# Kernel tuning notes

Measured on AMD Instinct MI355X. Metric: run time of the kernel, lower is better.

Reference implementation:

```python
import jax, jax.numpy as jnp
import numpy as np

N_NODES = 100000
N_EDGES = 1600000
D_FEAT = 128
UNITS = 128
LEAKY_ALPHA = 0.2  # tf.nn.leaky_relu default


def setup_inputs() -> dict:
    key = jax.random.key(0)
    k1, k2, k3, k4 = jax.random.split(key, 4)
    node_states = jax.random.normal(k1, (N_NODES, D_FEAT), dtype=jnp.float32)
    edges = jax.random.randint(k2, (N_EDGES, 2), 0, N_NODES, dtype=jnp.int64)
    kernel = jax.random.normal(k3, (D_FEAT, UNITS), dtype=jnp.float32) * (1.0 / np.sqrt(D_FEAT))
    kernel_attention = jax.random.normal(k4, (2 * UNITS, 1), dtype=jnp.float32) * (1.0 / np.sqrt(2 * UNITS))
    return {
        "node_states": node_states,
        "edges": edges,
        "kernel": kernel,
        "kernel_attention": kernel_attention,
    }


def reference(node_states, edges, kernel, kernel_attention):
    n = node_states.shape[0]
    tgt_idx = edges[:, 0]
    src_idx = edges[:, 1]

    # node_states_transformed: [N, units]
    h = node_states @ kernel

    # Attention logits. concat([tgt, src]) @ ka == tgt @ ka_t + src @ ka_s
    # (avoids materializing the [E, 2*units] concat).
    ka_t = kernel_attention[:UNITS, 0]   # [units]
    ka_s = kernel_attention[UNITS:, 0]   # [units]
    score_t = h @ ka_t                   # [N]
    score_s = h @ ka_s                   # [N]
    e = score_t[tgt_idx] + score_s[src_idx]              # [E]
    e = jax.nn.leaky_relu(e, negative_slope=LEAKY_ALPHA)
    e = jnp.exp(jnp.clip(e, -2.0, 2.0))

    # Segment softmax over incoming edges of each target node.
    sum_e = jax.ops.segment_sum(e, tgt_idx, num_segments=n)  # [N]
    attention = e / (sum_e[tgt_idx] + 1e-9)                  # [E]

    # Weighted scatter-sum of source messages.
    messages = h[src_idx] * attention[:, None]               # [E, units]
    output = jax.ops.segment_sum(messages, tgt_idx, num_segments=n)  # [N, units]
    return output
```

## Files before the change

kernel.cpp:

```cpp
#include <hip/hip_runtime.h>
#include <stdint.h>

typedef unsigned short ushort_t;
typedef __attribute__((ext_vector_type(8))) short short8;
typedef __attribute__((ext_vector_type(4))) float float4v;
typedef __attribute__((ext_vector_type(2))) float float2v;

#define N_NODES 100000
#define N_EDGES 1600000
#define D 128
#define NB_GEMM 1563
#define NBG     521
#define NB_B1   250
#define EPB     6400
#define BUCKETS 782
#define CAP     2560

static __device__ __forceinline__ float2v up2(uint32_t u) {
    float2v r;
    r.x = __builtin_bit_cast(float, u << 16);
    r.y = __builtin_bit_cast(float, u & 0xffff0000u);
    return r;
}
static __device__ __forceinline__ uint32_t f2bf_u(float f) {
    uint32_t u = __builtin_bit_cast(uint32_t, f);
    return (u + 0x7fffu + ((u >> 16) & 1u)) >> 16;
}
static __device__ __forceinline__ ushort_t f2bf(float f) {
    return (ushort_t)f2bf_u(f);
}
static __device__ __forceinline__ uint32_t pack2(float a, float b) {
    return f2bf_u(a) | (f2bf_u(b) << 16);
}
static __device__ __forceinline__ float edge_e(float s) {
    float x = (s >= 0.0f) ? s : 0.2f * s;
    x = fminf(fmaxf(x, -2.0f), 2.0f);
    return __expf(x);
}

__global__ void __launch_bounds__(256) fused_kernel(const float* __restrict__ X,
                                                    const float* __restrict__ W,
                                                    const float* __restrict__ KA,
                                                    ushort_t* __restrict__ H,
                                                    float* __restrict__ st,
                                                    float* __restrict__ ss,
                                                    int M,
                                                    const int* __restrict__ E,
                                                    int* __restrict__ sortedE,
                                                    ushort_t* __restrict__ bmat,
                                                    ushort_t* __restrict__ lofs) {
    __shared__ __align__(16) ushort_t lds_raw[16384];
    __shared__ float lds_wa[256];
    __shared__ int   ldet;
    int tid = threadIdx.x;
    if (blockIdx.x >= NBG) {
        int eb = blockIdx.x - NBG;
        int* lhist = (int*)lds_raw;
        int* lpart = ((int*)lds_raw) + 1024;
        int t = tid;
        if (t == 0) ldet = 0;
        for (int j = t; j < 1024; j += 256) lhist[j] = 0;
        __syncthreads();
        int nz = 0;
#pragma unroll
        for (int j = 0; j < 8; j++)
            if (E[(t + j * 256) * 2 + 1] != 0) nz = 1;
        if (nz) atomicOr(&ldet, 1);
        __syncthreads();
        int i64 = (ldet == 0) ? 1 : 0;
        int base = eb * EPB;
        int bin[25], w[25];
#pragma unroll
        for (int j = 0; j < 25; j++) {
            int i = base + j * 256 + t;
            int tgt, src;
            if (i64) { uint4 v = *(const uint4*)(E + (size_t)i * 4); tgt = (int)v.x; src = (int)v.z; }
            else     { uint2 v = *(const uint2*)(E + (size_t)i * 2); tgt = (int)v.x; src = (int)v.y; }
            if ((unsigned)tgt >= (unsigned)N_NODES) tgt = 0;
            if ((unsigned)src >= (unsigned)N_NODES) src = 0;
            bin[j] = tgt >> 7;
            w[j]   = ((tgt & 127) << 17) | src;
            atomicAdd(&lhist[bin[j]], 1);
        }
        __syncthreads();
        int c0 = lhist[t * 4], c1 = lhist[t * 4 + 1];
        int c2 = lhist[t * 4 + 2], c3 = lhist[t * 4 + 3];
        int sum = c0 + c1 + c2 + c3;
        lpart[t] = sum;
        __syncthreads();
        for (int off = 1; off < 256; off <<= 1) {
            int x = (t >= off) ? lpart[t - off] : 0;
            __syncthreads();
            lpart[t] += x;
            __syncthreads();
        }
        int e0 = lpart[t] - sum;
        int e1 = e0 + c0, e2 = e1 + c1, e3 = e2 + c2;
        int cc[4] = {c0, c1, c2, c3};
        int ee[4] = {e0, e1, e2, e3};
#pragma unroll
        for (int k = 0; k < 4; k++) {
            int bb = t * 4 + k;
            if (bb < BUCKETS) {
                bmat[eb * BUCKETS + bb] = (ushort_t)cc[k];
                lofs[eb * BUCKETS + bb] = (ushort_t)ee[k];
            }
        }
        lhist[t * 4] = e0; lhist[t * 4 + 1] = e1;
        lhist[t * 4 + 2] = e2; lhist[t * 4 + 3] = e3;
        __syncthreads();
#pragma unroll
        for (int j = 0; j < 25; j++) {
            int pos = atomicAdd(&lhist[bin[j]], 1);
            if (pos < EPB) sortedE[base + pos] = w[j];
        }
        return;
    }
    {
        const float4* W4 = (const float4*)W;
        for (int c = tid; c < 4096; c += 256) {
            float4 w4 = W4[c];
            int i0 = c * 4;
            int k = i0 >> 7;
            int kb = k >> 5, q = (k >> 3) & 3, jj = k & 7;
            const float* wp = (const float*)&w4;
#pragma unroll
            for (int u = 0; u < 4; u++) {
                int nn = (i0 + u) & 127;
                int tt = nn >> 4, l = nn & 15;
                lds_raw[((kb * 8 + tt) * 64 + q * 16 + l) * 8 + jj] = f2bf(wp[u]);
            }
        }
        int half = tid >> 7, k = tid & 127;
        const float* kav = KA + half * 128;
        const float* wrow = W + k * 128;
        float acc = 0.0f;
#pragma unroll 8
        for (int j = 0; j < 128; j++) acc += wrow[j] * kav[j];
        lds_wa[half * 128 + k] = acc;
    }
    __syncthreads();

    int wave = tid >> 6, lane = tid & 63;
    int quad = lane >> 4, l16 = lane & 15;
    int t0 = blockIdx.x;

    float4 f[8];
    {
        int ar = t0 * 64 + wave * 16 + l16; if (ar >= M) ar = M - 1;
        const float* xr = X + (size_t)ar * D + quad * 8;
#pragma unroll
        for (int kb = 0; kb < 4; kb++) {
            f[kb * 2]     = *(const float4*)(xr + kb * 32);
            f[kb * 2 + 1] = *(const float4*)(xr + kb * 32 + 4);
        }
    }
#pragma unroll
    for (int it = 0; it < 3; it++) {
        int m0 = (t0 + it * NBG) * 64 + wave * 16;
        float4 nf[8];
        if (it < 2) {
            int ar = (t0 + (it + 1) * NBG) * 64 + wave * 16 + l16;
            if (ar >= M) ar = M - 1;
            const float* xr = X + (size_t)ar * D + quad * 8;
#pragma unroll
            for (int kb = 0; kb < 4; kb++) {
                nf[kb * 2]     = *(const float4*)(xr + kb * 32);
                nf[kb * 2 + 1] = *(const float4*)(xr + kb * 32 + 4);
            }
        }
        short8 a[4];
        float sct = 0.0f, scs = 0.0f;
#pragma unroll
        for (int kb = 0; kb < 4; kb++) {
            float4 f0 = f[kb * 2], f1 = f[kb * 2 + 1];
            const float* wt0 = lds_wa + kb * 32 + quad * 8;
            float4 t0v = *(const float4*)(wt0);
            float4 t1v = *(const float4*)(wt0 + 4);
            float4 s0v = *(const float4*)(wt0 + 128);
            float4 s1v = *(const float4*)(wt0 + 132);
            sct += f0.x * t0v.x + f0.y * t0v.y + f0.z * t0v.z + f0.w * t0v.w
                 + f1.x * t1v.x + f1.y * t1v.y + f1.z * t1v.z + f1.w * t1v.w;
            scs += f0.x * s0v.x + f0.y * s0v.y + f0.z * s0v.z + f0.w * s0v.w
                 + f1.x * s1v.x + f1.y * s1v.y + f1.z * s1v.z + f1.w * s1v.w;
            short8 v;
            v[0] = (short)f2bf(f0.x); v[1] = (short)f2bf(f0.y);
            v[2] = (short)f2bf(f0.z); v[3] = (short)f2bf(f0.w);
            v[4] = (short)f2bf(f1.x); v[5] = (short)f2bf(f1.y);
            v[6] = (short)f2bf(f1.z); v[7] = (short)f2bf(f1.w);
            a[kb] = v;
        }
        sct += __shfl_xor(sct, 16); sct += __shfl_xor(sct, 32);
        scs += __shfl_xor(scs, 16); scs += __shfl_xor(scs, 32);
        if (quad == 0 && m0 + l16 < M) { st[m0 + l16] = sct; ss[m0 + l16] = scs; }

        float4v acc[8] = {};
#pragma unroll
        for (int kb = 0; kb < 4; kb++) {
#pragma unroll
            for (int t = 0; t < 8; t++) {
                short8 b = *(const short8*)(&lds_raw[((kb * 8 + t) * 64 + lane) * 8]);
                acc[t] = __builtin_amdgcn_mfma_f32_16x16x32_bf16(a[kb], b, acc[t], 0, 0, 0);
            }
        }
#pragma unroll
        for (int r = 0; r < 4; r++) {
            int orow = m0 + quad * 4 + r;
            if (orow < M) {
                uint4 v;
                v.x = pack2(acc[0][r], acc[1][r]);
                v.y = pack2(acc[2][r], acc[3][r]);
                v.z = pack2(acc[4][r], acc[5][r]);
                v.w = pack2(acc[6][r], acc[7][r]);
                *(uint4*)(H + (size_t)orow * D + l16 * 8) = v;
            }
        }
        if (it < 2) {
#pragma unroll
            for (int j = 0; j < 8; j++) f[j] = nf[j];
        }
    }
}

__global__ void __launch_bounds__(512) agg2_kernel(const ushort_t* __restrict__ bmat,
                                                   const ushort_t* __restrict__ lofs,
                                                   const int* __restrict__ sortedE,
                                                   const float* __restrict__ st,
                                                   const float* __restrict__ ss,
                                                   const ushort_t* __restrict__ H,
                                                   float* __restrict__ out) {
    __shared__ int stage[CAP];
    __shared__ int sortedLoc[CAP];
    __shared__ int lh[128];
    __shared__ int lrp[129];
    __shared__ int wsum[8];
    __shared__ int lsoff[NB_B1];
    __shared__ int lsst[NB_B1];
    int b = blockIdx.x >> 1, half = blockIdx.x & 1;
    int t = threadIdx.x;
    int lane = t & 63, wv = t >> 6;
    int cnt = 0, sst = 0;
    if (t < NB_B1) {
        cnt = bmat[t * BUCKETS + b];
        sst = lofs[t * BUCKETS + b];
    }
    int x = cnt;
#pragma unroll
    for (int off = 1; off < 64; off <<= 1) {
        int y = __shfl_up(x, off);
        if (lane >= off) x += y;
    }
    if (lane == 63) wsum[wv] = x;
    if (t < 128) lh[t] = 0;
    __syncthreads();
    int wbase = 0, total = 0;
#pragma unroll
    for (int w = 0; w < 8; w++) {
        int sv = wsum[w];
        if (w < wv) wbase += sv;
        total += sv;
    }
    if (total > CAP) total = CAP;
    int soff = wbase + x - cnt;
    if (t < NB_B1) { lsoff[t] = soff; lsst[t] = sst; }
    __syncthreads();
    for (int j = t; j < total; j += 512) {
        int lo = 0, hi = NB_B1 - 1;
        while (lo < hi) {
            int mid = (lo + hi + 1) >> 1;
            if (lsoff[mid] <= j) lo = mid; else hi = mid - 1;
        }
        stage[j] = sortedE[lo * EPB + lsst[lo] + (j - lsoff[lo])];
    }
    __syncthreads();
    for (int j = t; j < total; j += 512)
        atomicAdd(&lh[stage[j] >> 17], 1);
    __syncthreads();
    int v = (t < 128) ? lh[t] : 0;
    int xs = v;
#pragma unroll
    for (int off = 1; off < 64; off <<= 1) {
        int y = __shfl_up(xs, off);
        if (lane >= off) xs += y;
    }
    if (t == 63) wsum[0] = xs;
    __syncthreads();
    if (t < 128) {
        int inc = (wv == 1) ? xs + wsum[0] : xs;
        int ex = inc - v;
        lrp[t] = ex;
        lh[t]  = ex;
    }
    if (t == 0) lrp[128] = total;
    __syncthreads();
    for (int j = t; j < total; j += 512) {
        int p = stage[j];
        int pos = atomicAdd(&lh[p >> 17], 1);
        if (pos < total) sortedLoc[pos] = p & 0x1FFFF;
    }
    __syncthreads();
    int g = lane >> 4, l = lane & 15;
    for (int nd0 = wv; nd0 < 64; nd0 += 8) {
        int nd = half * 64 + nd0;
        int gnode = b * 128 + nd;
        if (gnode >= N_NODES) break;
        int start = lrp[nd], end = lrp[nd + 1];
        float stn = st[gnode];
        float den = 0.0f;
        float2v acc2[4] = {};
        int m = start + g;
        for (; m + 12 < end; m += 16) {
            int s0 = sortedLoc[m],     s1 = sortedLoc[m + 4];
            int s2 = sortedLoc[m + 8], s3 = sortedLoc[m + 12];
            float e0 = edge_e(stn + ss[s0]);
            float e1 = edge_e(stn + ss[s1]);
            float e2 = edge_e(stn + ss[s2]);
            float e3 = edge_e(stn + ss[s3]);
            den += (e0 + e1) + (e2 + e3);
            uint4 p0 = *(const uint4*)(H + ((unsigned)s0 << 7) + l * 8);
            uint4 p1 = *(const uint4*)(H + ((unsigned)s1 << 7) + l * 8);
            uint4 p2 = *(const uint4*)(H + ((unsigned)s2 << 7) + l * 8);
            uint4 p3 = *(const uint4*)(H + ((unsigned)s3 << 7) + l * 8);
            float2v E0 = {e0, e0}, E1 = {e1, e1}, E2 = {e2, e2}, E3 = {e3, e3};
            acc2[0] += E0 * up2(p0.x) + E1 * up2(p1.x) + E2 * up2(p2.x) + E3 * up2(p3.x);
            acc2[1] += E0 * up2(p0.y) + E1 * up2(p1.y) + E2 * up2(p2.y) + E3 * up2(p3.y);
            acc2[2] += E0 * up2(p0.z) + E1 * up2(p1.z) + E2 * up2(p2.z) + E3 * up2(p3.z);
            acc2[3] += E0 * up2(p0.w) + E1 * up2(p1.w) + E2 * up2(p2.w) + E3 * up2(p3.w);
        }
        for (; m + 4 < end; m += 8) {
            int s0 = sortedLoc[m], s1 = sortedLoc[m + 4];
            float e0 = edge_e(stn + ss[s0]);
            float e1 = edge_e(stn + ss[s1]);
            den += e0 + e1;
            uint4 p0 = *(const uint4*)(H + ((unsigned)s0 << 7) + l * 8);
            uint4 p1 = *(const uint4*)(H + ((unsigned)s1 << 7) + l * 8);
            float2v E0 = {e0, e0}, E1 = {e1, e1};
            acc2[0] += E0 * up2(p0.x) + E1 * up2(p1.x);
            acc2[1] += E0 * up2(p0.y) + E1 * up2(p1.y);
            acc2[2] += E0 * up2(p0.z) + E1 * up2(p1.z);
            acc2[3] += E0 * up2(p0.w) + E1 * up2(p1.w);
        }
        if (m < end) {
            int s0 = sortedLoc[m];
            float e0 = edge_e(stn + ss[s0]);
            den += e0;
            uint4 p0 = *(const uint4*)(H + ((unsigned)s0 << 7) + l * 8);
            float2v E0 = {e0, e0};
            acc2[0] += E0 * up2(p0.x);
            acc2[1] += E0 * up2(p0.y);
            acc2[2] += E0 * up2(p0.z);
            acc2[3] += E0 * up2(p0.w);
        }
        den += __shfl_xor(den, 16);
        den += __shfl_xor(den, 32);
        float r[8];
#pragma unroll
        for (int j = 0; j < 4; j++) {
            float a0 = acc2[j].x, a1 = acc2[j].y;
            a0 += __shfl_xor(a0, 16); a0 += __shfl_xor(a0, 32);
            a1 += __shfl_xor(a1, 16); a1 += __shfl_xor(a1, 32);
            r[j * 2] = a0; r[j * 2 + 1] = a1;
        }
        float inv = 1.0f / (den + 1e-9f);
        if (g == 0) {
#pragma unroll
            for (int k = 0; k < 8; k++)
                out[(size_t)gnode * D + k * 16 + l] = r[k] * inv;
        }
    }
}

extern "C" void kernel_launch(void* const* d_in, const int* in_sizes, int n_in,
                              void* d_out, int out_size, void* d_ws, size_t ws_size,
                              hipStream_t stream) {
    const float* X  = (const float*)d_in[0];
    const int*   E  = (const int*)d_in[1];
    const float* W  = (const float*)d_in[2];
    const float* KA = (const float*)d_in[3];
    for (int i = 0; i < n_in; i++) {
        int s = in_sizes[i];
        if (s == N_NODES * D)      X  = (const float*)d_in[i];
        else if (s == N_EDGES * 2) E  = (const int*)d_in[i];
        else if (s == D * D)       W  = (const float*)d_in[i];
        else if (s == 2 * D)       KA = (const float*)d_in[i];
    }
    float* out = (float*)d_out;

    char* ws = (char*)d_ws;
    ushort_t* H        = (ushort_t*)(ws + 0);
    float*    st       = (float*)   (ws + 25601024);
    float*    ssb      = (float*)   (ws + 26001024);
    int*      sortedE  = (int*)     (ws + 26401024);
    ushort_t* bmat     = (ushort_t*)(ws + 32801024);
    ushort_t* lofs     = (ushort_t*)(ws + 33192032);

    fused_kernel<<<NBG + NB_B1, 256, 0, stream>>>(X, W, KA, H, st, ssb,
                                                  N_NODES, E,
                                                  sortedE, bmat, lofs);
    agg2_kernel<<<2 * BUCKETS, 512, 0, stream>>>(bmat, lofs, sortedE, st, ssb,
                                                 H, out);
}
```

Before: 214.9 us.

## Use 64-node buckets with larger edge windows and two-pass edge bucketing

The edge bucketing now uses 64-node target buckets and 12800-edge windows, so there are 125 sort blocks feeding 1563 aggregation blocks. Each aggregation block now handles a whole bucket, which drops the previous half-bucket split where two blocks redundantly staged and sorted the same 128-node bucket. The sort pass re-reads edges in a second loop instead of holding them in registers, and per-bucket counts are stored as bytes. A small vectorised float4 dot product for the W·KA projection is also added. The trade-offs are an extra read of the edge array, and byte counts that would overflow if a bucket received more than 255 edges from one window.

```diff
diff --git a/kernel.cpp b/kernel.cpp
--- a/kernel.cpp
+++ b/kernel.cpp
@@ -2,6 +2,7 @@
 #include <stdint.h>
 
 typedef unsigned short ushort_t;
+typedef unsigned char uchar_t;
 typedef __attribute__((ext_vector_type(8))) short short8;
 typedef __attribute__((ext_vector_type(4))) float float4v;
 typedef __attribute__((ext_vector_type(2))) float float2v;
@@ -11,10 +12,10 @@
 #define D 128
 #define NB_GEMM 1563
 #define NBG     521
-#define NB_B1   250
-#define EPB     6400
-#define BUCKETS 782
-#define CAP     2560
+#define NWIN    125
+#define EPB     12800
+#define NBUCK   1563
+#define CAP     1280
 
 static __device__ __forceinline__ float2v up2(uint32_t u) {
     float2v r;
@@ -47,7 +48,7 @@
                                                     int M,
                                                     const int* __restrict__ E,
                                                     int* __restrict__ sortedE,
-                                                    ushort_t* __restrict__ bmat,
+                                                    uchar_t* __restrict__ bmat,
                                                     ushort_t* __restrict__ lofs) {
     __shared__ __align__(16) ushort_t lds_raw[16384];
     __shared__ float lds_wa[256];
@@ -56,10 +57,10 @@
     if (blockIdx.x >= NBG) {
         int eb = blockIdx.x - NBG;
         int* lhist = (int*)lds_raw;
-        int* lpart = ((int*)lds_raw) + 1024;
+        int* lpart = ((int*)lds_raw) + 2048;
         int t = tid;
         if (t == 0) ldet = 0;
-        for (int j = t; j < 1024; j += 256) lhist[j] = 0;
+        for (int j = t; j < 2048; j += 256) lhist[j] = 0;
         __syncthreads();
         int nz = 0;
 #pragma unroll
@@ -69,50 +70,48 @@
         __syncthreads();
         int i64 = (ldet == 0) ? 1 : 0;
         int base = eb * EPB;
-        int bin[25], w[25];
-#pragma unroll
-        for (int j = 0; j < 25; j++) {
+        for (int j = 0; j < 50; j++) {
+            int i = base + j * 256 + t;
+            int tgt = i64 ? E[(size_t)i * 4] : E[(size_t)i * 2];
+            if ((unsigned)tgt >= (unsigned)N_NODES) tgt = 0;
+            atomicAdd(&lhist[tgt >> 6], 1);
+        }
+        __syncthreads();
+        int c[8], sum = 0;
+#pragma unroll
+        for (int k = 0; k < 8; k++) { c[k] = lhist[t * 8 + k]; sum += c[k]; }
+        lpart[t] = sum;
+        __syncthreads();
+        for (int off = 1; off < 256; off <<= 1) {
+            int x = (t >= off) ? lpart[t - off] : 0;
+            __syncthreads();
+            lpart[t] += x;
+            __syncthreads();
+        }
+        int e = lpart[t] - sum;
+        int ee[8];
+#pragma unroll
+        for (int k = 0; k < 8; k++) { ee[k] = e; e += c[k]; }
+#pragma unroll
+        for (int k = 0; k < 8; k++) {
+            int bb = t * 8 + k;
+            if (bb < NBUCK) {
+                bmat[eb * NBUCK + bb] = (uchar_t)c[k];
+                lofs[eb * NBUCK + bb] = (ushort_t)ee[k];
+            }
+        }
+#pragma unroll
+        for (int k = 0; k < 8; k++) lhist[t * 8 + k] = ee[k];
+        __syncthreads();
+        for (int j = 0; j < 50; j++) {
             int i = base + j * 256 + t;
             int tgt, src;
             if (i64) { uint4 v = *(const uint4*)(E + (size_t)i * 4); tgt = (int)v.x; src = (int)v.z; }
             else     { uint2 v = *(const uint2*)(E + (size_t)i * 2); tgt = (int)v.x; src = (int)v.y; }
             if ((unsigned)tgt >= (unsigned)N_NODES) tgt = 0;
             if ((unsigned)src >= (unsigned)N_NODES) src = 0;
-            bin[j] = tgt >> 7;
-            w[j]   = ((tgt & 127) << 17) | src;
-            atomicAdd(&lhist[bin[j]], 1);
-        }
-        __syncthreads();
-        int c0 = lhist[t * 4], c1 = lhist[t * 4 + 1];
-        int c2 = lhist[t * 4 + 2], c3 = lhist[t * 4 + 3];
-        int sum = c0 + c1 + c2 + c3;
-        lpart[t] = sum;
-        __syncthreads();
-        for (int off = 1; off < 256; off <<= 1) {
-            int x = (t >= off) ? lpart[t - off] : 0;
-            __syncthreads();
-            lpart[t] += x;
-            __syncthreads();
-        }
-        int e0 = lpart[t] - sum;
-        int e1 = e0 + c0, e2 = e1 + c1, e3 = e2 + c2;
-        int cc[4] = {c0, c1, c2, c3};
-        int ee[4] = {e0, e1, e2, e3};
-#pragma unroll
-        for (int k = 0; k < 4; k++) {
-            int bb = t * 4 + k;
-            if (bb < BUCKETS) {
-                bmat[eb * BUCKETS + bb] = (ushort_t)cc[k];
-                lofs[eb * BUCKETS + bb] = (ushort_t)ee[k];
-            }
-        }
-        lhist[t * 4] = e0; lhist[t * 4 + 1] = e1;
-        lhist[t * 4 + 2] = e2; lhist[t * 4 + 3] = e3;
-        __syncthreads();
-#pragma unroll
-        for (int j = 0; j < 25; j++) {
-            int pos = atomicAdd(&lhist[bin[j]], 1);
-            if (pos < EPB) sortedE[base + pos] = w[j];
+            int pos = atomicAdd(&lhist[tgt >> 6], 1);
+            if (pos < EPB) sortedE[base + pos] = ((tgt & 63) << 17) | src;
         }
         return;
     }
@@ -132,11 +131,14 @@
             }
         }
         int half = tid >> 7, k = tid & 127;
-        const float* kav = KA + half * 128;
-        const float* wrow = W + k * 128;
+        const float4* kav4  = (const float4*)(KA + half * 128);
+        const float4* wrow4 = (const float4*)(W + (size_t)k * 128);
         float acc = 0.0f;
 #pragma unroll 8
-        for (int j = 0; j < 128; j++) acc += wrow[j] * kav[j];
+        for (int j = 0; j < 32; j++) {
+            float4 a4 = wrow4[j], b4 = kav4[j];
+            acc += a4.x * b4.x + a4.y * b4.y + a4.z * b4.z + a4.w * b4.w;
+        }
         lds_wa[half * 128 + k] = acc;
     }
     __syncthreads();
@@ -222,7 +224,7 @@
     }
 }
 
-__global__ void __launch_bounds__(512) agg2_kernel(const ushort_t* __restrict__ bmat,
+__global__ void __launch_bounds__(512) agg2_kernel(const uchar_t* __restrict__ bmat,
                                                    const ushort_t* __restrict__ lofs,
                                                    const int* __restrict__ sortedE,
                                                    const float* __restrict__ st,
@@ -231,18 +233,17 @@
                                                    float* __restrict__ out) {
     __shared__ int stage[CAP];
     __shared__ int sortedLoc[CAP];
-    __shared__ int lh[128];
-    __shared__ int lrp[129];
+    __shared__ int lh[64];
+    __shared__ int lrp[65];
     __shared__ int wsum[8];
-    __shared__ int lsoff[NB_B1];
-    __shared__ int lsst[NB_B1];
-    int b = blockIdx.x >> 1, half = blockIdx.x & 1;
-    int t = threadIdx.x;
+    __shared__ int lsoff[NWIN];
+    __shared__ int lsst[NWIN];
+    int b = blockIdx.x, t = threadIdx.x;
     int lane = t & 63, wv = t >> 6;
     int cnt = 0, sst = 0;
-    if (t < NB_B1) {
-        cnt = bmat[t * BUCKETS + b];
-        sst = lofs[t * BUCKETS + b];
+    if (t < NWIN) {
+        cnt = bmat[t * NBUCK + b];
+        sst = lofs[t * NBUCK + b];
     }
     int x = cnt;
 #pragma unroll
@@ -251,7 +252,7 @@
         if (lane >= off) x += y;
     }
     if (lane == 63) wsum[wv] = x;
-    if (t < 128) lh[t] = 0;
+    if (t < 64) lh[t] = 0;
     __syncthreads();
     int wbase = 0, total = 0;
 #pragma unroll
@@ -262,10 +263,10 @@
     }
     if (total > CAP) total = CAP;
     int soff = wbase + x - cnt;
-    if (t < NB_B1) { lsoff[t] = soff; lsst[t] = sst; }
+    if (t < NWIN) { lsoff[t] = soff; lsst[t] = sst; }
     __syncthreads();
     for (int j = t; j < total; j += 512) {
-        int lo = 0, hi = NB_B1 - 1;
+        int lo = 0, hi = NWIN - 1;
         while (lo < hi) {
             int mid = (lo + hi + 1) >> 1;
             if (lsoff[mid] <= j) lo = mid; else hi = mid - 1;
@@ -276,22 +277,19 @@
     for (int j = t; j < total; j += 512)
         atomicAdd(&lh[stage[j] >> 17], 1);
     __syncthreads();
-    int v = (t < 128) ? lh[t] : 0;
-    int xs = v;
-#pragma unroll
-    for (int off = 1; off < 64; off <<= 1) {
-        int y = __shfl_up(xs, off);
-        if (lane >= off) xs += y;
-    }
-    if (t == 63) wsum[0] = xs;
-    __syncthreads();
-    if (t < 128) {
-        int inc = (wv == 1) ? xs + wsum[0] : xs;
-        int ex = inc - v;
+    if (t < 64) {
+        int v = lh[t];
+        int xs = v;
+#pragma unroll
+        for (int off = 1; off < 64; off <<= 1) {
+            int y = __shfl_up(xs, off);
+            if (lane >= off) xs += y;
+        }
+        int ex = xs - v;
         lrp[t] = ex;
         lh[t]  = ex;
     }
-    if (t == 0) lrp[128] = total;
+    if (t == 0) lrp[64] = total;
     __syncthreads();
     for (int j = t; j < total; j += 512) {
         int p = stage[j];
@@ -300,9 +298,8 @@
     }
     __syncthreads();
     int g = lane >> 4, l = lane & 15;
-    for (int nd0 = wv; nd0 < 64; nd0 += 8) {
-        int nd = half * 64 + nd0;
-        int gnode = b * 128 + nd;
+    for (int nd = wv; nd < 64; nd += 8) {
+        int gnode = b * 64 + nd;
         if (gnode >= N_NODES) break;
         int start = lrp[nd], end = lrp[nd + 1];
         float stn = st[gnode];
@@ -388,15 +385,15 @@
 
     char* ws = (char*)d_ws;
     ushort_t* H        = (ushort_t*)(ws + 0);
-    float*    st       = (float*)   (ws + 25601024);
-    float*    ssb      = (float*)   (ws + 26001024);
-    int*      sortedE  = (int*)     (ws + 26401024);
-    ushort_t* bmat     = (ushort_t*)(ws + 32801024);
-    ushort_t* lofs     = (ushort_t*)(ws + 33192032);
-
-    fused_kernel<<<NBG + NB_B1, 256, 0, stream>>>(X, W, KA, H, st, ssb,
-                                                  N_NODES, E,
-                                                  sortedE, bmat, lofs);
-    agg2_kernel<<<2 * BUCKETS, 512, 0, stream>>>(bmat, lofs, sortedE, st, ssb,
-                                                 H, out);
-}
+    float*    st       = (float*)   (ws + 25600000);
+    float*    ssb      = (float*)   (ws + 26000000);
+    int*      sortedE  = (int*)     (ws + 26400000);
+    ushort_t* lofs     = (ushort_t*)(ws + 32800000);
+    uchar_t*  bmat     = (uchar_t*) (ws + 33190752);
+
+    fused_kernel<<<NBG + NWIN, 256, 0, stream>>>(X, W, KA, H, st, ssb,
+                                                 N_NODES, E,
+                                                 sortedE, bmat, lofs);
+    agg2_kernel<<<NBUCK, 512, 0, stream>>>(bmat, lofs, sortedE, st, ssb,
+                                           H, out);
+}
```

Result: slower. 232.2 us (+8.1%).

## Use one GEMM tile per block and one aggregation block per bucket

Applied to the files above, without the earlier changes.

The GEMM phase of the fused kernel now launches one block per 64-row tile instead of 521 blocks each looping over three tiles with software prefetch. The W-to-LDS transpose is rewritten so each thread builds a full short8 with one vector LDS store, and the W·ka dot uses float4 loads. The aggregation kernel drops the two-blocks-per-bucket split, so each bucket's edge staging and sort runs once per bucket instead of twice. The trade-off is more per-block W setup for the GEMM and fewer, longer aggregation blocks with less parallelism.

```diff
diff --git a/kernel.cpp b/kernel.cpp
--- a/kernel.cpp
+++ b/kernel.cpp
@@ -10,8 +10,7 @@
 #define N_EDGES 1600000
 #define D 128
 #define NB_GEMM 1563
-#define NBG     521
-#define NB_B1   250
+#define NWIN    250
 #define EPB     6400
 #define BUCKETS 782
 #define CAP     2560
@@ -53,8 +52,8 @@
     __shared__ float lds_wa[256];
     __shared__ int   ldet;
     int tid = threadIdx.x;
-    if (blockIdx.x >= NBG) {
-        int eb = blockIdx.x - NBG;
+    if (blockIdx.x >= NB_GEMM) {
+        int eb = blockIdx.x - NB_GEMM;
         int* lhist = (int*)lds_raw;
         int* lpart = ((int*)lds_raw) + 1024;
         int t = tid;
@@ -117,37 +116,36 @@
         return;
     }
     {
-        const float4* W4 = (const float4*)W;
-        for (int c = tid; c < 4096; c += 256) {
-            float4 w4 = W4[c];
-            int i0 = c * 4;
-            int k = i0 >> 7;
-            int kb = k >> 5, q = (k >> 3) & 3, jj = k & 7;
-            const float* wp = (const float*)&w4;
-#pragma unroll
-            for (int u = 0; u < 4; u++) {
-                int nn = (i0 + u) & 127;
-                int tt = nn >> 4, l = nn & 15;
-                lds_raw[((kb * 8 + tt) * 64 + q * 16 + l) * 8 + jj] = f2bf(wp[u]);
-            }
+        for (int c = tid; c < 2048; c += 256) {
+            int l = c & 15, q = (c >> 4) & 3, tt = (c >> 6) & 7, kb = c >> 9;
+            int n = tt * 16 + l;
+            int k0 = kb * 32 + q * 8;
+            short8 v;
+#pragma unroll
+            for (int jj = 0; jj < 8; jj++)
+                v[jj] = (short)f2bf(W[(size_t)(k0 + jj) * 128 + n]);
+            *(short8*)(&lds_raw[((kb * 8 + tt) * 64 + q * 16 + l) * 8]) = v;
         }
         int half = tid >> 7, k = tid & 127;
-        const float* kav = KA + half * 128;
-        const float* wrow = W + k * 128;
+        const float4* kav4  = (const float4*)(KA + half * 128);
+        const float4* wrow4 = (const float4*)(W + (size_t)k * 128);
         float acc = 0.0f;
 #pragma unroll 8
-        for (int j = 0; j < 128; j++) acc += wrow[j] * kav[j];
+        for (int j = 0; j < 32; j++) {
+            float4 a4 = wrow4[j], b4 = kav4[j];
+            acc += a4.x * b4.x + a4.y * b4.y + a4.z * b4.z + a4.w * b4.w;
+        }
         lds_wa[half * 128 + k] = acc;
     }
     __syncthreads();
 
     int wave = tid >> 6, lane = tid & 63;
     int quad = lane >> 4, l16 = lane & 15;
-    int t0 = blockIdx.x;
+    int m0 = blockIdx.x * 64 + wave * 16;
 
     float4 f[8];
     {
-        int ar = t0 * 64 + wave * 16 + l16; if (ar >= M) ar = M - 1;
+        int ar = m0 + l16; if (ar >= M) ar = M - 1;
         const float* xr = X + (size_t)ar * D + quad * 8;
 #pragma unroll
         for (int kb = 0; kb < 4; kb++) {
@@ -155,69 +153,50 @@
             f[kb * 2 + 1] = *(const float4*)(xr + kb * 32 + 4);
         }
     }
-#pragma unroll
-    for (int it = 0; it < 3; it++) {
-        int m0 = (t0 + it * NBG) * 64 + wave * 16;
-        float4 nf[8];
-        if (it < 2) {
-            int ar = (t0 + (it + 1) * NBG) * 64 + wave * 16 + l16;
-            if (ar >= M) ar = M - 1;
-            const float* xr = X + (size_t)ar * D + quad * 8;
-#pragma unroll
-            for (int kb = 0; kb < 4; kb++) {
-                nf[kb * 2]     = *(const float4*)(xr + kb * 32);
-                nf[kb * 2 + 1] = *(const float4*)(xr + kb * 32 + 4);
-            }
-        }
-        short8 a[4];
-        float sct = 0.0f, scs = 0.0f;
-#pragma unroll
-        for (int kb = 0; kb < 4; kb++) {
-            float4 f0 = f[kb * 2], f1 = f[kb * 2 + 1];
-            const float* wt0 = lds_wa + kb * 32 + quad * 8;
-            float4 t0v = *(const float4*)(wt0);
-            float4 t1v = *(const float4*)(wt0 + 4);
-            float4 s0v = *(const float4*)(wt0 + 128);
-            float4 s1v = *(const float4*)(wt0 + 132);
-            sct += f0.x * t0v.x + f0.y * t0v.y + f0.z * t0v.z + f0.w * t0v.w
-                 + f1.x * t1v.x + f1.y * t1v.y + f1.z * t1v.z + f1.w * t1v.w;
-            scs += f0.x * s0v.x + f0.y * s0v.y + f0.z * s0v.z + f0.w * s0v.w
-                 + f1.x * s1v.x + f1.y * s1v.y + f1.z * s1v.z + f1.w * s1v.w;
-            short8 v;
-            v[0] = (short)f2bf(f0.x); v[1] = (short)f2bf(f0.y);
-            v[2] = (short)f2bf(f0.z); v[3] = (short)f2bf(f0.w);
-            v[4] = (short)f2bf(f1.x); v[5] = (short)f2bf(f1.y);
-            v[6] = (short)f2bf(f1.z); v[7] = (short)f2bf(f1.w);
-            a[kb] = v;
-        }
-        sct += __shfl_xor(sct, 16); sct += __shfl_xor(sct, 32);
-        scs += __shfl_xor(scs, 16); scs += __shfl_xor(scs, 32);
-        if (quad == 0 && m0 + l16 < M) { st[m0 + l16] = sct; ss[m0 + l16] = scs; }
-
-        float4v acc[8] = {};
-#pragma unroll
-        for (int kb = 0; kb < 4; kb++) {
-#pragma unroll
-            for (int t = 0; t < 8; t++) {
-                short8 b = *(const short8*)(&lds_raw[((kb * 8 + t) * 64 + lane) * 8]);
-                acc[t] = __builtin_amdgcn_mfma_f32_16x16x32_bf16(a[kb], b, acc[t], 0, 0, 0);
-            }
-        }
-#pragma unroll
-        for (int r = 0; r < 4; r++) {
-            int orow = m0 + quad * 4 + r;
-            if (orow < M) {
-                uint4 v;
-                v.x = pack2(acc[0][r], acc[1][r]);
-                v.y = pack2(acc[2][r], acc[3][r]);
-                v.z = pack2(acc[4][r], acc[5][r]);
-                v.w = pack2(acc[6][r], acc[7][r]);
-                *(uint4*)(H + (size_t)orow * D + l16 * 8) = v;
-            }
-        }
-        if (it < 2) {
-#pragma unroll
-            for (int j = 0; j < 8; j++) f[j] = nf[j];
+    short8 a[4];
+    float sct = 0.0f, scs = 0.0f;
+#pragma unroll
+    for (int kb = 0; kb < 4; kb++) {
+        float4 f0 = f[kb * 2], f1 = f[kb * 2 + 1];
+        const float* wt0 = lds_wa + kb * 32 + quad * 8;
+        float4 t0v = *(const float4*)(wt0);
+        float4 t1v = *(const float4*)(wt0 + 4);
+        float4 s0v = *(const float4*)(wt0 + 128);
+        float4 s1v = *(const float4*)(wt0 + 132);
+        sct += f0.x * t0v.x + f0.y * t0v.y + f0.z * t0v.z + f0.w * t0v.w
+             + f1.x * t1v.x + f1.y * t1v.y + f1.z * t1v.z + f1.w * t1v.w;
+        scs += f0.x * s0v.x + f0.y * s0v.y + f0.z * s0v.z + f0.w * s0v.w
+             + f1.x * s1v.x + f1.y * s1v.y + f1.z * s1v.z + f1.w * s1v.w;
+        short8 v;
+        v[0] = (short)f2bf(f0.x); v[1] = (short)f2bf(f0.y);
+        v[2] = (short)f2bf(f0.z); v[3] = (short)f2bf(f0.w);
+        v[4] = (short)f2bf(f1.x); v[5] = (short)f2bf(f1.y);
+        v[6] = (short)f2bf(f1.z); v[7] = (short)f2bf(f1.w);
+        a[kb] = v;
+    }
+    sct += __shfl_xor(sct, 16); sct += __shfl_xor(sct, 32);
+    scs += __shfl_xor(scs, 16); scs += __shfl_xor(scs, 32);
+    if (quad == 0 && m0 + l16 < M) { st[m0 + l16] = sct; ss[m0 + l16] = scs; }
+
+    float4v acc[8] = {};
+#pragma unroll
+    for (int kb = 0; kb < 4; kb++) {
+#pragma unroll
+        for (int t = 0; t < 8; t++) {
+            short8 b = *(const short8*)(&lds_raw[((kb * 8 + t) * 64 + lane) * 8]);
+            acc[t] = __builtin_amdgcn_mfma_f32_16x16x32_bf16(a[kb], b, acc[t], 0, 0, 0);
+        }
+    }
+#pragma unroll
+    for (int r = 0; r < 4; r++) {
+        int orow = m0 + quad * 4 + r;
+        if (orow < M) {
+            uint4 v;
+            v.x = pack2(acc[0][r], acc[1][r]);
+            v.y = pack2(acc[2][r], acc[3][r]);
+            v.z = pack2(acc[4][r], acc[5][r]);
+            v.w = pack2(acc[6][r], acc[7][r]);
+            *(uint4*)(H + (size_t)orow * D + l16 * 8) = v;
         }
     }
 }
@@ -234,13 +213,12 @@
     __shared__ int lh[128];
     __shared__ int lrp[129];
     __shared__ int wsum[8];
-    __shared__ int lsoff[NB_B1];
-    __shared__ int lsst[NB_B1];
-    int b = blockIdx.x >> 1, half = blockIdx.x & 1;
-    int t = threadIdx.x;
+    __shared__ int lsoff[NWIN];
+    __shared__ int lsst[NWIN];
+    int b = blockIdx.x, t = threadIdx.x;
     int lane = t & 63, wv = t >> 6;
     int cnt = 0, sst = 0;
-    if (t < NB_B1) {
+    if (t < NWIN) {
         cnt = bmat[t * BUCKETS + b];
         sst = lofs[t * BUCKETS + b];
     }
@@ -262,10 +240,10 @@
     }
     if (total > CAP) total = CAP;
     int soff = wbase + x - cnt;
-    if (t < NB_B1) { lsoff[t] = soff; lsst[t] = sst; }
+    if (t < NWIN) { lsoff[t] = soff; lsst[t] = sst; }
     __syncthreads();
     for (int j = t; j < total; j += 512) {
-        int lo = 0, hi = NB_B1 - 1;
+        int lo = 0, hi = NWIN - 1;
         while (lo < hi) {
             int mid = (lo + hi + 1) >> 1;
             if (lsoff[mid] <= j) lo = mid; else hi = mid - 1;
@@ -300,8 +278,7 @@
     }
     __syncthreads();
     int g = lane >> 4, l = lane & 15;
-    for (int nd0 = wv; nd0 < 64; nd0 += 8) {
-        int nd = half * 64 + nd0;
+    for (int nd = wv; nd < 128; nd += 8) {
         int gnode = b * 128 + nd;
         if (gnode >= N_NODES) break;
         int start = lrp[nd], end = lrp[nd + 1];
@@ -394,9 +371,9 @@
     ushort_t* bmat     = (ushort_t*)(ws + 32801024);
     ushort_t* lofs     = (ushort_t*)(ws + 33192032);
 
-    fused_kernel<<<NBG + NB_B1, 256, 0, stream>>>(X, W, KA, H, st, ssb,
-                                                  N_NODES, E,
-                                                  sortedE, bmat, lofs);
-    agg2_kernel<<<2 * BUCKETS, 512, 0, stream>>>(bmat, lofs, sortedE, st, ssb,
-                                                 H, out);
-}
+    fused_kernel<<<NB_GEMM + NWIN, 256, 0, stream>>>(X, W, KA, H, st, ssb,
+                                                     N_NODES, E,
+                                                     sortedE, bmat, lofs);
+    agg2_kernel<<<BUCKETS, 512, 0, stream>>>(bmat, lofs, sortedE, st, ssb,
+                                             H, out);
+}
```

After: 227.2 us. 5.7% more time.
